# Performance work log

Measured on AMD Instinct MI355X. Metric: run time of the kernel, lower is better.

## Reference

```python
import jax, jax.numpy as jnp
import numpy as np

KH, KW = 3, 3  # kernel size (stride 1, SAME padding, rate 1)


def extract_patches_same(x, kh, kw):
    """TF tf.image.extract_patches, stride 1, rate 1, SAME padding (zero pad).
    x: [B,H,W,C] -> [B,H,W,kh*kw,C], patch ordered (ki, kj) row-major like TF."""
    B, H, W, C = x.shape
    ph, pw = (kh - 1) // 2, (kw - 1) // 2  # TF SAME: pad_before = (k-1)//2 for stride 1
    xp = jnp.pad(x, ((0, 0), (ph, kh - 1 - ph), (pw, kw - 1 - pw), (0, 0)))
    patches = jnp.stack(
        [xp[:, i:i + H, j:j + W, :] for i in range(kh) for j in range(kw)], axis=3
    )
    return patches  # [B,H,W,P,C] with P = kh*kw


def max_times_plus_p4(x, kernel, times_kernel):
    """x: [B,H,W,Cin]; kernel, times_kernel: [kh,kw,Cin,F].
    out[b,r,i,j,f] = sum_c max_p (patch[b,i,j,p,c]*tK_rot[p,c,f] + K_rot[p,c,f])."""
    kh, kw = kernel.shape[0], kernel.shape[1]
    patches = extract_patches_same(x, kh, kw)  # [B,H,W,P,C]
    res = []
    for r in range(4):  # 4 P4 rotations of the structuring elements
        k_rot = jnp.rot90(kernel, k=r, axes=(0, 1)).reshape(kh * kw, kernel.shape[2], kernel.shape[3])
        t_rot = jnp.rot90(times_kernel, k=r, axes=(0, 1)).reshape(kh * kw, kernel.shape[2], kernel.shape[3])
        # tropical (max-times-plus) lifting: mult-add then max over patch, sum over channel
        z = patches[..., None] * t_rot + k_rot          # [B,H,W,P,C,F]
        res.append(jnp.sum(jnp.max(z, axis=3), axis=3))  # [B,H,W,F]
    return jnp.stack(res, axis=1)  # [B,4,H,W,F]


def setup_inputs() -> dict:
    key = jax.random.key(0)
    k1, k2, k3 = jax.random.split(key, 3)
    B, H, W, Cin, F = 4, 64, 64, 16, 32
    x = jax.random.normal(k1, (B, H, W, Cin), dtype=jnp.float32)
    kernel = jax.random.normal(k2, (KH, KW, Cin, F), dtype=jnp.float32)
    times_kernel = jax.random.uniform(k3, (KH, KW, Cin, F), dtype=jnp.float32)  # NonNeg constraint
    return {"x": x, "kernel": kernel, "times_kernel": times_kernel}


def reference(x, kernel, times_kernel):
    return max_times_plus_p4(x, kernel, times_kernel)
```

## Files before the change

### kernel.cpp

```cpp
#include <hip/hip_runtime.h>

#define B_  4
#define H_  64
#define W_  64
#define C_  16
#define F_  32

#define NWE (8 * 9 * F_)
#define NXE (3 * 34 * 4)

__global__ __launch_bounds__(512, 4) void mtp_main(const float* __restrict__ x,
                                                   const float* __restrict__ kern,
                                                   const float* __restrict__ tker,
                                                   float* __restrict__ out) {
    __shared__ float4 wlds[NWE];
    __shared__ float2 xlds[3][34][8];

    const int tid  = threadIdx.x;
    const int bidx = blockIdx.x;
    const int half = bidx & 1;
    const int i    = (bidx >> 1) & 63;
    const int b    = bidx >> 7;

    for (int e = tid; e < NWE; e += 512) {
        int f  = e & 31;
        int t  = e >> 5;
        int q  = t % 9;
        int cc = t / 9;
        int s0 = (q * C_ + cc * 2 + 0) * F_ + f;
        int s1 = (q * C_ + cc * 2 + 1) * F_ + f;
        wlds[e] = make_float4(tker[s0], tker[s1], kern[s0], kern[s1]);
    }
    for (int e = tid; e < NXE; e += 512) {
        int cc4 = e & 3;
        int t   = e >> 2;
        int cl  = t % 34;
        int di  = t / 34;
        int ro  = i + di - 1;
        int co  = half * 32 + cl - 1;
        float4 v = make_float4(0.f, 0.f, 0.f, 0.f);
        if (ro >= 0 && ro < H_ && co >= 0 && co < W_)
            v = *reinterpret_cast<const float4*>(
                    x + ((b * H_ + ro) * W_ + co) * C_ + cc4 * 4);
        *reinterpret_cast<float4*>(&xlds[di][cl][cc4 * 2]) = v;
    }
    __syncthreads();

    const int lane = tid & 63;
    const int f    = lane & 31;
    const int ps   = lane >> 5;
    const int w    = tid >> 6;
    const int jb_l = w << 2;

    float acc[4][2];
    #pragma unroll
    for (int r = 0; r < 4; ++r) { acc[r][0] = 0.f; acc[r][1] = 0.f; }

    #pragma unroll 1
    for (int cc = 0; cc < 8; ++cc) {
        float4 wq[9];
        #pragma unroll
        for (int q = 0; q < 9; ++q)
            wq[q] = wlds[(cc * 9 + q) * F_ + f];
        float2 xh[3][5];
        #pragma unroll
        for (int di = 0; di < 3; ++di)
            #pragma unroll
            for (int lc = 0; lc < 5; ++lc)
                xh[di][lc] = xlds[di][jb_l + ps + lc][cc];

        #pragma unroll
        for (int it = 0; it < 2; ++it) {
            #pragma unroll
            for (int r = 0; r < 4; ++r) {
                float z0[9], z1[9];
                #pragma unroll
                for (int q = 0; q < 9; ++q) {
                    const int a = q / 3, bq = q % 3;
                    int di, dj;
                    switch (r) {
                        case 0:  di = a;      dj = bq;     break;
                        case 1:  di = 2 - bq; dj = a;      break;
                        case 2:  di = 2 - a;  dj = 2 - bq; break;
                        default: di = bq;     dj = 2 - a;  break;
                    }
                    const float2 xv = xh[di][it * 2 + dj];
                    z0[q] = fmaf(xv.x, wq[q].x, wq[q].z);
                    z1[q] = fmaf(xv.y, wq[q].y, wq[q].w);
                }
                float m0 = fmaxf(fmaxf(fmaxf(z0[0], z0[1]), z0[2]),
                           fmaxf(fmaxf(fmaxf(z0[3], z0[4]), z0[5]),
                                 fmaxf(fmaxf(z0[6], z0[7]), z0[8])));
                float m1 = fmaxf(fmaxf(fmaxf(z1[0], z1[1]), z1[2]),
                           fmaxf(fmaxf(fmaxf(z1[3], z1[4]), z1[5]),
                                 fmaxf(fmaxf(z1[6], z1[7]), z1[8])));
                acc[r][it] += m0 + m1;
            }
        }
    }

    const int jg = half * 32 + jb_l + ps;
    #pragma unroll
    for (int r = 0; r < 4; ++r) {
        float* op = out + ((((b * 4 + r) * H_ + i) * W_ + jg) * F_ + f);
        op[0]      = acc[r][0];
        op[2 * F_] = acc[r][1];
    }
}

extern "C" void kernel_launch(void* const* d_in, const int* in_sizes, int n_in,
                              void* d_out, int out_size, void* d_ws, size_t ws_size,
                              hipStream_t stream) {
    const float* x    = (const float*)d_in[0];
    const float* kern = (const float*)d_in[1];
    const float* tker = (const float*)d_in[2];
    float* out = (float*)d_out;

    hipLaunchKernelGGL(mtp_main, dim3(B_ * H_ * 2), dim3(512), 0, stream,
                       x, kern, tker, out);
}
```

Baseline: 19.20 us.

## Drop x LDS staging, read input from global and double per-thread output columns

Removes the shared-memory staging of the input tile and has each thread load its 3x9 neighbourhood of x directly from global memory, with clamped addresses and zeroing for the borders. Each block now covers a full image row instead of half a row, so the grid is halved and every thread produces four output columns per rotation instead of two. The weight LDS fill is unrolled, and the occupancy hint is removed from launch bounds. This saves LDS traffic and one sync path, and it amortises the weight staging over more outputs. In exchange it uses more registers, relies on cache for the global loads, and launches only 256 blocks, which may underfill the GPU.

```diff
diff --git a/kernel.cpp b/kernel.cpp
--- a/kernel.cpp
+++ b/kernel.cpp
@@ -7,42 +7,30 @@
 #define F_  32
 
 #define NWE (8 * 9 * F_)
-#define NXE (3 * 34 * 4)
 
-__global__ __launch_bounds__(512, 4) void mtp_main(const float* __restrict__ x,
-                                                   const float* __restrict__ kern,
-                                                   const float* __restrict__ tker,
-                                                   float* __restrict__ out) {
+__global__ __launch_bounds__(512) void mtp_main(const float* __restrict__ x,
+                                                const float* __restrict__ kern,
+                                                const float* __restrict__ tker,
+                                                float* __restrict__ out) {
     __shared__ float4 wlds[NWE];
-    __shared__ float2 xlds[3][34][8];
 
     const int tid  = threadIdx.x;
     const int bidx = blockIdx.x;
-    const int half = bidx & 1;
-    const int i    = (bidx >> 1) & 63;
-    const int b    = bidx >> 7;
+    const int i    = bidx & 63;
+    const int b    = bidx >> 6;
 
-    for (int e = tid; e < NWE; e += 512) {
-        int f  = e & 31;
-        int t  = e >> 5;
-        int q  = t % 9;
-        int cc = t / 9;
-        int s0 = (q * C_ + cc * 2 + 0) * F_ + f;
-        int s1 = (q * C_ + cc * 2 + 1) * F_ + f;
-        wlds[e] = make_float4(tker[s0], tker[s1], kern[s0], kern[s1]);
-    }
-    for (int e = tid; e < NXE; e += 512) {
-        int cc4 = e & 3;
-        int t   = e >> 2;
-        int cl  = t % 34;
-        int di  = t / 34;
-        int ro  = i + di - 1;
-        int co  = half * 32 + cl - 1;
-        float4 v = make_float4(0.f, 0.f, 0.f, 0.f);
-        if (ro >= 0 && ro < H_ && co >= 0 && co < W_)
-            v = *reinterpret_cast<const float4*>(
-                    x + ((b * H_ + ro) * W_ + co) * C_ + cc4 * 4);
-        *reinterpret_cast<float4*>(&xlds[di][cl][cc4 * 2]) = v;
+    #pragma unroll
+    for (int e0 = 0; e0 < 5; ++e0) {
+        int e = e0 * 512 + tid;
+        if (e < NWE) {
+            int f  = e & 31;
+            int t  = e >> 5;
+            int q  = t % 9;
+            int cc = t / 9;
+            int s0 = (q * C_ + cc * 2 + 0) * F_ + f;
+            int s1 = (q * C_ + cc * 2 + 1) * F_ + f;
+            wlds[e] = make_float4(tker[s0], tker[s1], kern[s0], kern[s1]);
+        }
     }
     __syncthreads();
 
@@ -50,11 +38,25 @@
     const int f    = lane & 31;
     const int ps   = lane >> 5;
     const int w    = tid >> 6;
-    const int jb_l = w << 2;
+    const int jb   = w << 3;
+    const int col0 = jb + ps - 1;
 
-    float acc[4][2];
+    const bool okL = (col0 >= 0);
+    const bool okR = (col0 + 8 <= 63);
+    const bool ok0 = (i > 0);
+    const bool ok2 = (i < 63);
+    const int colL = okL ? col0 : 0;
+    const int colR = okR ? col0 + 8 : 63;
+
+    const float* rowp0 = x + ((b * H_ + (ok0 ? i - 1 : 0)) * W_) * C_;
+    const float* rowp1 = x + ((b * H_ + i) * W_) * C_;
+    const float* rowp2 = x + ((b * H_ + (ok2 ? i + 1 : 0)) * W_) * C_;
+
+    float acc[4][4];
     #pragma unroll
-    for (int r = 0; r < 4; ++r) { acc[r][0] = 0.f; acc[r][1] = 0.f; }
+    for (int r = 0; r < 4; ++r)
+        #pragma unroll
+        for (int it = 0; it < 4; ++it) acc[r][it] = 0.f;
 
     #pragma unroll 1
     for (int cc = 0; cc < 8; ++cc) {
@@ -62,15 +64,33 @@
         #pragma unroll
         for (int q = 0; q < 9; ++q)
             wq[q] = wlds[(cc * 9 + q) * F_ + f];
-        float2 xh[3][5];
+
+        float2 xh[3][9];
+        const float* rp[3] = { rowp0, rowp1, rowp2 };
         #pragma unroll
-        for (int di = 0; di < 3; ++di)
+        for (int dr = 0; dr < 3; ++dr) {
+            const float* rb = rp[dr];
+            const float* bm = rb + (col0 + 1) * C_ + cc * 2;
+            xh[dr][0] = *reinterpret_cast<const float2*>(rb + colL * C_ + cc * 2);
             #pragma unroll
-            for (int lc = 0; lc < 5; ++lc)
-                xh[di][lc] = xlds[di][jb_l + ps + lc][cc];
+            for (int h = 1; h <= 7; ++h)
+                xh[dr][h] = *reinterpret_cast<const float2*>(bm + (h - 1) * C_);
+            xh[dr][8] = *reinterpret_cast<const float2*>(rb + colR * C_ + cc * 2);
+        }
+        const float2 z2 = make_float2(0.f, 0.f);
+        if (!okL) { xh[0][0] = z2; xh[1][0] = z2; xh[2][0] = z2; }
+        if (!okR) { xh[0][8] = z2; xh[1][8] = z2; xh[2][8] = z2; }
+        if (!ok0) {
+            #pragma unroll
+            for (int h = 0; h < 9; ++h) xh[0][h] = z2;
+        }
+        if (!ok2) {
+            #pragma unroll
+            for (int h = 0; h < 9; ++h) xh[2][h] = z2;
+        }
 
         #pragma unroll
-        for (int it = 0; it < 2; ++it) {
+        for (int it = 0; it < 4; ++it) {
             #pragma unroll
             for (int r = 0; r < 4; ++r) {
                 float z0[9], z1[9];
@@ -99,12 +119,12 @@
         }
     }
 
-    const int jg = half * 32 + jb_l + ps;
     #pragma unroll
     for (int r = 0; r < 4; ++r) {
-        float* op = out + ((((b * 4 + r) * H_ + i) * W_ + jg) * F_ + f);
-        op[0]      = acc[r][0];
-        op[2 * F_] = acc[r][1];
+        float* op = out + ((((b * 4 + r) * H_ + i) * W_ + jb + ps) * F_ + f);
+        #pragma unroll
+        for (int it = 0; it < 4; ++it)
+            op[it * 2 * F_] = acc[r][it];
     }
 }
 
@@ -116,6 +136,6 @@
     const float* tker = (const float*)d_in[2];
     float* out = (float*)d_out;
 
-    hipLaunchKernelGGL(mtp_main, dim3(B_ * H_ * 2), dim3(512), 0, stream,
+    hipLaunchKernelGGL(mtp_main, dim3(B_ * H_), dim3(512), 0, stream,
                        x, kern, tker, out);
 }
```

After: 22.06 us. +14.9%, slower.

## Split channel pairs across half-waves and compute four pixels per thread

Applied to the files above, without the earlier changes.

Each wave now splits the channel reduction between its two 32-lane halves, and every thread computes four adjacent output pixels for its half of the channels. The halves are combined with a cross-lane shuffle before the store. This lets each loaded weight and input window be reused across more pixels, cutting LDS reads per FLOP and halving the channel-loop trip count. The cost is more accumulators and registers. The launch-bounds occupancy hint is also dropped, which may change register allocation.

```diff
diff --git a/kernel.cpp b/kernel.cpp
--- a/kernel.cpp
+++ b/kernel.cpp
@@ -9,10 +9,10 @@
 #define NWE (8 * 9 * F_)
 #define NXE (3 * 34 * 4)
 
-__global__ __launch_bounds__(512, 4) void mtp_main(const float* __restrict__ x,
-                                                   const float* __restrict__ kern,
-                                                   const float* __restrict__ tker,
-                                                   float* __restrict__ out) {
+__global__ __launch_bounds__(512) void mtp_main(const float* __restrict__ x,
+                                                const float* __restrict__ kern,
+                                                const float* __restrict__ tker,
+                                                float* __restrict__ out) {
     __shared__ float4 wlds[NWE];
     __shared__ float2 xlds[3][34][8];
 
@@ -23,12 +23,12 @@
     const int b    = bidx >> 7;
 
     for (int e = tid; e < NWE; e += 512) {
-        int f  = e & 31;
-        int t  = e >> 5;
-        int q  = t % 9;
-        int cc = t / 9;
-        int s0 = (q * C_ + cc * 2 + 0) * F_ + f;
-        int s1 = (q * C_ + cc * 2 + 1) * F_ + f;
+        int f   = e & 31;
+        int t   = e >> 5;
+        int q   = t % 9;
+        int ccp = t / 9;
+        int s0 = (q * C_ + ccp * 2 + 0) * F_ + f;
+        int s1 = (q * C_ + ccp * 2 + 1) * F_ + f;
         wlds[e] = make_float4(tker[s0], tker[s1], kern[s0], kern[s1]);
     }
     for (int e = tid; e < NXE; e += 512) {
@@ -48,29 +48,36 @@
 
     const int lane = tid & 63;
     const int f    = lane & 31;
-    const int ps   = lane >> 5;
+    const int g    = lane >> 5;
     const int w    = tid >> 6;
-    const int jb_l = w << 2;
+    const int w4   = w << 2;
 
-    float acc[4][2];
+    float acc[4][4];
     #pragma unroll
-    for (int r = 0; r < 4; ++r) { acc[r][0] = 0.f; acc[r][1] = 0.f; }
+    for (int px = 0; px < 4; ++px)
+        #pragma unroll
+        for (int r = 0; r < 4; ++r) acc[px][r] = 0.f;
+
+    const int wbase = g * (4 * 9 * F_) + f;
 
     #pragma unroll 1
-    for (int cc = 0; cc < 8; ++cc) {
+    for (int it = 0; it < 4; ++it) {
+        const int pidx = g * 4 + it;
+
         float4 wq[9];
         #pragma unroll
         for (int q = 0; q < 9; ++q)
-            wq[q] = wlds[(cc * 9 + q) * F_ + f];
-        float2 xh[3][5];
+            wq[q] = wlds[wbase + (it * 9 + q) * F_];
+
+        float2 xh[3][6];
         #pragma unroll
-        for (int di = 0; di < 3; ++di)
+        for (int dr = 0; dr < 3; ++dr)
             #pragma unroll
-            for (int lc = 0; lc < 5; ++lc)
-                xh[di][lc] = xlds[di][jb_l + ps + lc][cc];
+            for (int lc = 0; lc < 6; ++lc)
+                xh[dr][lc] = xlds[dr][w4 + lc][pidx];
 
         #pragma unroll
-        for (int it = 0; it < 2; ++it) {
+        for (int px = 0; px < 4; ++px) {
             #pragma unroll
             for (int r = 0; r < 4; ++r) {
                 float z0[9], z1[9];
@@ -84,7 +91,7 @@
                         case 2:  di = 2 - a;  dj = 2 - bq; break;
                         default: di = bq;     dj = 2 - a;  break;
                     }
-                    const float2 xv = xh[di][it * 2 + dj];
+                    const float2 xv = xh[di][px + dj];
                     z0[q] = fmaf(xv.x, wq[q].x, wq[q].z);
                     z1[q] = fmaf(xv.y, wq[q].y, wq[q].w);
                 }
@@ -94,17 +101,26 @@
                 float m1 = fmaxf(fmaxf(fmaxf(z1[0], z1[1]), z1[2]),
                            fmaxf(fmaxf(fmaxf(z1[3], z1[4]), z1[5]),
                                  fmaxf(fmaxf(z1[6], z1[7]), z1[8])));
-                acc[r][it] += m0 + m1;
+                acc[px][r] += m0 + m1;
             }
         }
     }
 
-    const int jg = half * 32 + jb_l + ps;
+    float tot[4][4];
+    #pragma unroll
+    for (int px = 0; px < 4; ++px)
+        #pragma unroll
+        for (int r = 0; r < 4; ++r)
+            tot[px][r] = acc[px][r] + __shfl_xor(acc[px][r], 32, 64);
+
+    const int jg = half * 32 + w4 + g;
     #pragma unroll
     for (int r = 0; r < 4; ++r) {
         float* op = out + ((((b * 4 + r) * H_ + i) * W_ + jg) * F_ + f);
-        op[0]      = acc[r][0];
-        op[2 * F_] = acc[r][1];
+        float v0 = g ? tot[1][r] : tot[0][r];
+        float v1 = g ? tot[3][r] : tot[2][r];
+        op[0]      = v0;
+        op[2 * F_] = v1;
     }
 }
 
```

After: 21.28 us. +10.9%, slower.
